# Optimization experiments

Hardware: AMD Instinct MI355X
Metric: run time of the kernel (lower is better)

The kernel has to match this reference:

```python
import jax, jax.numpy as jnp
import numpy as np

# Model dims
C = 16          # in_channels / d_model
D_INNER = 64    # expand * C, expand = 64 // C = 4
HEADDIM = 4
NHEADS = D_INNER // HEADDIM   # 16
D_STATE = 64
D_CONV = 4
CONV_DIM = D_INNER + 2 * D_STATE        # 192 (x, B, C streams)
D_IN_PROJ = 2 * D_INNER + 2 * D_STATE + NHEADS  # 272 (z, xBC, dt)
# Input volume
BSZ, DD, HH, WW = 8, 32, 16, 16
L = DD * HH * WW  # 8192, multiple of 256 -> exact adaptive max pool
POOL = 256


def setup_inputs():
    key = jax.random.key(0)
    ks = jax.random.split(key, 10)
    x = jax.random.normal(ks[0], (BSZ, C, DD, HH, WW), jnp.float32)
    # 3 independent Mamba2 blocks -> stack params with leading dim 3
    Win = jax.random.normal(ks[1], (3, D_IN_PROJ, C), jnp.float32) / np.sqrt(C).astype(np.float32)
    conv_w = jax.random.normal(ks[2], (3, CONV_DIM, D_CONV), jnp.float32) / np.sqrt(D_CONV).astype(np.float32)
    conv_b = jax.random.normal(ks[3], (3, CONV_DIM), jnp.float32) * 0.1
    dt_bias = jax.random.normal(ks[4], (3, NHEADS), jnp.float32) * 0.5
    A_log = jnp.log(jax.random.uniform(ks[5], (3, NHEADS), jnp.float32, minval=1.0, maxval=16.0))
    Dp = jax.random.normal(ks[6], (3, NHEADS), jnp.float32) * 0.5 + 1.0
    norm_w = jnp.ones((3, D_INNER), jnp.float32)
    Wout = jax.random.normal(ks[7], (3, C, D_INNER), jnp.float32) / np.sqrt(D_INNER).astype(np.float32)
    gamma = jnp.ones((3, C), jnp.float32)
    beta = jnp.zeros((3, C), jnp.float32)
    lin_w = jax.random.normal(ks[8], (3, 1, C), jnp.float32) / np.sqrt(C).astype(np.float32)
    lin_b = jnp.zeros((3, 1), jnp.float32)
    return dict(x=x, Win=Win, conv_w=conv_w, conv_b=conv_b, dt_bias=dt_bias,
                A_log=A_log, Dp=Dp, norm_w=norm_w, Wout=Wout,
                gamma=gamma, beta=beta, lin_w=lin_w, lin_b=lin_b)


def _mamba2(u, Win, conv_w, conv_b, dt_bias, A_log, Dp, norm_w, Wout):
    """Mamba2 block: u (B, L, C) -> (B, L, C). ngroups=1, rmsnorm gated."""
    B, Lx, _ = u.shape
    zxbcdt = jnp.einsum('blc,pc->blp', u, Win)  # (B, L, 272)
    z = zxbcdt[..., :D_INNER]
    xBC = zxbcdt[..., D_INNER:D_INNER + CONV_DIM]
    dt = jax.nn.softplus(zxbcdt[..., D_INNER + CONV_DIM:] + dt_bias)  # (B, L, H)
    # causal depthwise conv over time
    conv = jax.lax.conv_general_dilated(
        jnp.transpose(xBC, (0, 2, 1)), conv_w[:, None, :], (1,),
        [(D_CONV - 1, 0)], feature_group_count=CONV_DIM)
    xBC = jax.nn.silu(jnp.transpose(conv, (0, 2, 1)) + conv_b)
    xh = xBC[..., :D_INNER].reshape(B, Lx, NHEADS, HEADDIM)
    Bm = xBC[..., D_INNER:D_INNER + D_STATE]   # (B, L, N)
    Cm = xBC[..., D_INNER + D_STATE:]          # (B, L, N)
    A = -jnp.exp(A_log)                        # (H,)
    dA = jnp.exp(dt * A)                       # (B, L, H)
    dtx = dt[..., None] * xh                   # (B, L, H, P)

    def step(S, inp):
        dA_t, dtx_t, B_t, C_t = inp
        S = S * dA_t[:, :, None, None] + dtx_t[..., None] * B_t[:, None, None, :]
        y_t = jnp.einsum('bhpn,bn->bhp', S, C_t)
        return S, y_t

    S0 = jnp.zeros((B, NHEADS, HEADDIM, D_STATE), u.dtype)
    xs = (jnp.moveaxis(dA, 1, 0), jnp.moveaxis(dtx, 1, 0),
          jnp.moveaxis(Bm, 1, 0), jnp.moveaxis(Cm, 1, 0))
    _, ys = jax.lax.scan(step, S0, xs)                       # (L, B, H, P)
    y = jnp.moveaxis(ys, 0, 1) + Dp[None, None, :, None] * xh
    y = y.reshape(B, Lx, D_INNER) * jax.nn.silu(z)           # gate first
    y = y * jax.lax.rsqrt(jnp.mean(y * y, -1, keepdims=True) + 1e-5) * norm_w
    return jnp.einsum('bld,cd->blc', y, Wout)


def _proj_pool(y, gamma, beta, lw, lb):
    """ReLU -> BatchNorm1d (batch stats) -> Linear(C,1) -> AdaptiveMaxPool1d(256)."""
    B, Lx, _ = y.shape
    v = jax.nn.relu(y.reshape(-1, C))
    mu = jnp.mean(v, 0)
    var = jnp.mean((v - mu) ** 2, 0)
    v = (v - mu) * jax.lax.rsqrt(var + 1e-5) * gamma + beta
    s = (v @ lw.T + lb).reshape(B, Lx)
    return jnp.max(s.reshape(B, POOL, Lx // POOL), -1)  # (B, 256)


def reference(x, Win, conv_w, conv_b, dt_bias, A_log, Dp, norm_w, Wout,
              gamma, beta, lin_w, lin_b):
    B, Cc, Dd, Hh, Ww = x.shape
    Lx = Dd * Hh * Ww
    fD = jnp.transpose(x.reshape(B, Cc, Lx), (0, 2, 1))
    fH = jnp.transpose(jnp.transpose(x, (0, 1, 3, 4, 2)).reshape(B, Cc, Lx), (0, 2, 1))
    fW = jnp.transpose(jnp.transpose(x, (0, 1, 4, 2, 3)).reshape(B, Cc, Lx), (0, 2, 1))
    seqs = jnp.stack([fD, fH, fW], 0)  # (3, B, L, C)
    ys = jax.vmap(_mamba2)(seqs, Win, conv_w, conv_b, dt_bias, A_log, Dp, norm_w, Wout)
    pooled = jax.vmap(_proj_pool)(ys, gamma, beta, lin_w, lin_b)  # (3, B, 256)
    return jnp.concatenate([pooled[0], pooled[1], pooled[2]], -1)[:, None, :]  # (B,1,768)
```

## Files before the change

kernel.cpp:

```cpp
#include <hip/hip_runtime.h>
#include <math.h>

#define CONVD 192
#define NC 128
#define PW 32
#define LOG2E 1.4426950408889634f
#define LN2f  0.69314718055994531f

#define OFF_DST   0u
#define OFF_CHA   4194304u
#define OFF_YS    4210688u
#define OFF_PART  5259264u
#define PD        5292032u

#define XSW(m, t)   ((m) * 64 + (((((t) >> 2) ^ ((m) & 15)) & 15) << 2) + ((t) & 3))
#define XSW4(m, tq) ((m) * 64 + ((((tq) ^ ((m) & 15)) & 15) << 2))

__device__ __forceinline__ float fast_silu(float x) {
    float e = __builtin_amdgcn_exp2f(-x * LOG2E);
    return x * __builtin_amdgcn_rcpf(1.f + e);
}
__device__ __forceinline__ float fast_softplus(float x) {
    if (x > 20.f) return x;
    float e = __builtin_amdgcn_exp2f(x * LOG2E);
    return LN2f * __builtin_amdgcn_logf(1.f + e);
}

template<int NT>
__device__ __forceinline__ void stage_u(
    const float* __restrict__ x, float* u_s, int b, int l0, int dir, int tid)
{
    for (int i = tid; i < 67 * 16; i += NT) {
        int pos = i >> 4, c = i & 15;
        int l = l0 + pos - 3;
        float v = 0.f;
        if (l >= 0) {
            if (dir == 0) {
                v = x[(b * 16 + c) * 8192 + l];
            } else if (dir == 1) {
                int h = l >> 9, w = (l >> 5) & 15, d = l & 31;
                v = x[(((b * 16 + c) * 32 + d) * 16 + h) * 16 + w];
            } else {
                int w = l >> 9, d = (l >> 4) & 31, h = l & 15;
                v = x[(((b * 16 + c) * 32 + d) * 16 + h) * 16 + w];
            }
        }
        u_s[pos * 17 + c] = v;
    }
}

__global__ __launch_bounds__(512, 6) void k_delta(
    const float* __restrict__ x, const float* __restrict__ Win,
    const float* __restrict__ convw, const float* __restrict__ convb,
    const float* __restrict__ dtb, const float* __restrict__ A_log,
    float* __restrict__ ws, int dir0, int dslm)
{
    __shared__ float u_s[67 * 17];
    __shared__ float xh_c[4096];
    __shared__ float Bs[4096];
    __shared__ float dts[16 * 65];
    __shared__ float wbuf[16 * 65];
    const int tid = threadIdx.x;
    const int ck = blockIdx.x;
    const int b = blockIdx.y;
    const int dir = dir0 + blockIdx.z;
    float* base = ws + (size_t)(dslm * blockIdx.z) * PD;
    float* Dst = base + OFF_DST;
    float* chA = base + OFF_CHA;
    const int l0 = ck * 64;

    stage_u<512>(x, u_s, b, l0, dir, tid);
    __syncthreads();

    const int lane = tid & 63;
    const int wv = __builtin_amdgcn_readfirstlane(tid >> 6);

    float u[16], uh[16];
    {
        const float* ur = &u_s[(lane + 3) * 17];
        #pragma unroll
        for (int k = 0; k < 16; k++) u[k] = ur[k];
        const float* uhr = &u_s[(lane < 3 ? lane : 0) * 17];
        #pragma unroll
        for (int k = 0; k < 16; k++) uh[k] = uhr[k];
    }

    for (int i = 0; i < 18; i++) {
        const int g = wv * 18 + i;
        const int col = (g < 128) ? (64 + g) : (256 + (g - 128));
        const float* wp = Win + (size_t)(dir * 272 + col) * 16;
        float acc = 0.f, hacc = 0.f;
        #pragma unroll
        for (int k = 0; k < 16; k++) {
            acc += u[k] * wp[k];
            hacc += uh[k] * wp[k];
        }
        if (col < 256) {
            const int ch = col - 64;
            float v1 = __shfl_up(acc, 1);
            float v2 = __shfl_up(acc, 2);
            float v3 = __shfl_up(acc, 3);
            float h0 = __shfl(hacc, 0);
            float h1 = __shfl(hacc, 1);
            float h2 = __shfl(hacc, 2);
            float m1 = (lane >= 1) ? v1 : h2;
            float m2 = (lane >= 2) ? v2 : ((lane == 0) ? h1 : h2);
            float m3 = (lane >= 3) ? v3 : ((lane == 0) ? h0 : ((lane == 1) ? h1 : h2));
            const float* cwp = convw + (size_t)(dir * CONVD + ch) * 4;
            float conv = convb[dir * CONVD + ch]
                       + cwp[0] * m3 + cwp[1] * m2 + cwp[2] * m1 + cwp[3] * acc;
            float xv = fast_silu(conv);
            if (ch < 64) xh_c[XSW(ch, lane)] = xv;
            else         Bs[XSW(ch - 64, lane)] = xv;
        } else {
            const int h = col - 256;
            dts[h * 65 + lane] = fast_softplus(acc + dtb[dir * 16 + h]);
        }
    }
    __syncthreads();

    for (int h = wv; h < 16; h += 8) {
        float A2 = -expf(A_log[dir * 16 + h]) * LOG2E;
        float dtv = dts[h * 65 + lane];
        float v = dtv * A2;
        #pragma unroll
        for (int off = 1; off < 64; off <<= 1) {
            float o = __shfl_up(v, off, 64);
            if (lane >= off) v += o;
        }
        float tot = __shfl(v, 63, 64);
        wbuf[h * 65 + lane] = __builtin_amdgcn_exp2f(tot - v) * dtv;
        if (lane == 63) chA[(b * 16 + h) * 128 + ck] = __builtin_amdgcn_exp2f(tot);
    }
    __syncthreads();

    for (int j = tid; j < 4096; j += 512) {
        int hp = j >> 6, t = j & 63;
        xh_c[XSW(hp, t)] *= wbuf[(hp >> 2) * 65 + t];
    }
    __syncthreads();

    if (tid < 256) {
        const int hp4 = tid >> 4, n4 = tid & 15;
        float a[4][4] = {};
        for (int tq = 0; tq < 16; tq++) {
            float4 xv[4], bv[4];
            #pragma unroll
            for (int i2 = 0; i2 < 4; i2++) {
                xv[i2] = *(const float4*)&xh_c[XSW4(4 * hp4 + i2, tq)];
                bv[i2] = *(const float4*)&Bs[XSW4(4 * n4 + i2, tq)];
            }
            #pragma unroll
            for (int i2 = 0; i2 < 4; i2++)
                #pragma unroll
                for (int j2 = 0; j2 < 4; j2++)
                    a[i2][j2] += xv[i2].x * bv[j2].x + xv[i2].y * bv[j2].y
                               + xv[i2].z * bv[j2].z + xv[i2].w * bv[j2].w;
        }
        #pragma unroll
        for (int i2 = 0; i2 < 4; i2++) {
            int hp = 4 * hp4 + i2;
            int h = hp >> 2, p = hp & 3;
            *(float4*)(Dst + ((size_t)((b * 16 + h) * 128 + ck)) * 256 + p * 64 + 4 * n4) =
                make_float4(a[i2][0], a[i2][1], a[i2][2], a[i2][3]);
        }
    }
}

__global__ __launch_bounds__(64) void k_chunk_scan(
    float* __restrict__ ws, int dslm)
{
    float* base = ws + (size_t)(dslm * blockIdx.z) * PD;
    float* Dst = base + OFF_DST;
    const float* chA = base + OFF_CHA;
    const int bh = blockIdx.x >> 2;
    const int elem = (blockIdx.x & 3) * 64 + threadIdx.x;
    float S = 0.f;
    for (int k0 = 0; k0 < NC; k0 += 8) {
        float d[8], av[8];
        #pragma unroll
        for (int j = 0; j < 8; j++) {
            d[j] = Dst[((size_t)(bh * 128 + k0 + j)) * 256 + elem];
            av[j] = chA[bh * 128 + k0 + j];
        }
        #pragma unroll
        for (int j = 0; j < 8; j++) {
            Dst[((size_t)(bh * 128 + k0 + j)) * 256 + elem] = S;
            S = av[j] * S + d[j];
        }
    }
}

__global__ __launch_bounds__(512, 4) void k_out_epi(
    const float* __restrict__ x, const float* __restrict__ Win,
    const float* __restrict__ convw, const float* __restrict__ convb,
    const float* __restrict__ dtb, const float* __restrict__ A_log,
    const float* __restrict__ Dp, const float* __restrict__ normw,
    const float* __restrict__ Wout, float* __restrict__ ws, int dir0, int dslm)
{
    __shared__ float SinT[64 * 65];
    __shared__ float xh_c[4096];
    __shared__ float Bz[4096];
    __shared__ float Cy[4352];
    __shared__ float uW[67 * 17];
    __shared__ float dts[16 * 68];
    __shared__ float ct2l[16 * 68];
    __shared__ float Dps[16];
    __shared__ float red[4][34];
    float* base = ws + (size_t)(dslm * blockIdx.z) * PD;
    const float* Dst = base + OFF_DST;
    float* ys        = base + OFF_YS;
    float* partials  = base + OFF_PART;
    const int dir = dir0 + blockIdx.z;
    const int tid = threadIdx.x;
    const int b = blockIdx.y;
    const int ck = blockIdx.x;
    const int l0 = ck * 64;
    const int tg = tid & 255;
    const int t4 = tg >> 4, x4 = tg & 15;
    const int grp = tid >> 8;
    const int lane = tid & 63;
    const int wv = __builtin_amdgcn_readfirstlane(tid >> 6);

    stage_u<512>(x, uW, b, l0, dir, tid);
    for (int j = tid; j < 1024; j += 512) {
        int hp = j >> 4, n4 = (j & 15) << 2;
        int h = hp >> 2, p = hp & 3;
        float4 sv = *(const float4*)(Dst + ((size_t)((b * 16 + h) * 128 + ck)) * 256 + p * 64 + n4);
        SinT[(n4 + 0) * 65 + hp] = sv.x;
        SinT[(n4 + 1) * 65 + hp] = sv.y;
        SinT[(n4 + 2) * 65 + hp] = sv.z;
        SinT[(n4 + 3) * 65 + hp] = sv.w;
    }
    if (tid < 16) Dps[tid] = Dp[dir * 16 + tid];
    __syncthreads();

    float u[16], uh[16];
    {
        const float* ur = &uW[(lane + 3) * 17];
        #pragma unroll
        for (int k = 0; k < 16; k++) u[k] = ur[k];
        const float* uhr = &uW[(lane < 3 ? lane : 0) * 17];
        #pragma unroll
        for (int k = 0; k < 16; k++) uh[k] = uhr[k];
    }

    for (int i = 0; i < 26; i++) {
        const int col = 64 + wv * 26 + i;
        const float* wp = Win + (size_t)(dir * 272 + col) * 16;
        float acc = 0.f, hacc = 0.f;
        #pragma unroll
        for (int k = 0; k < 16; k++) {
            acc += u[k] * wp[k];
            hacc += uh[k] * wp[k];
        }
        if (col < 256) {
            const int ch = col - 64;
            float v1 = __shfl_up(acc, 1);
            float v2 = __shfl_up(acc, 2);
            float v3 = __shfl_up(acc, 3);
            float h0 = __shfl(hacc, 0);
            float h1 = __shfl(hacc, 1);
            float h2 = __shfl(hacc, 2);
            float m1 = (lane >= 1) ? v1 : h2;
            float m2 = (lane >= 2) ? v2 : ((lane == 0) ? h1 : h2);
            float m3 = (lane >= 3) ? v3 : ((lane == 0) ? h0 : ((lane == 1) ? h1 : h2));
            const float* cwp = convw + (size_t)(dir * CONVD + ch) * 4;
            float conv = convb[dir * CONVD + ch]
                       + cwp[0] * m3 + cwp[1] * m2 + cwp[2] * m1 + cwp[3] * acc;
            float xv = fast_silu(conv);
            if (ch < 64)       xh_c[XSW(ch, lane)] = xv;
            else if (ch < 128) Bz[XSW(ch - 64, lane)] = xv;
            else               Cy[XSW(ch - 128, lane)] = xv;
        } else {
            const int h = col - 256;
            dts[h * 68 + lane] = fast_softplus(acc + dtb[dir * 16 + h]);
        }
    }
    __syncthreads();

    for (int h = wv; h < 16; h += 8) {
        float A2 = -expf(A_log[dir * 16 + h]) * LOG2E;
        float dtv = dts[h * 68 + lane];
        float v = dtv * A2;
        #pragma unroll
        for (int off = 1; off < 64; off <<= 1) {
            float o = __shfl_up(v, off, 64);
            if (lane >= off) v += o;
        }
        ct2l[h * 68 + lane] = v;
    }
    __syncthreads();

    float G_[4][4] = {}, CS_[4][4] = {};
    if (grp == 0) {
        for (int n = 0; n < 64; n++) {
            float4 cr4 = *(const float4*)&Cy[XSW4(n, t4)];
            float4 br4 = *(const float4*)&Bz[XSW4(n, x4)];
            float cr[4] = {cr4.x, cr4.y, cr4.z, cr4.w};
            float br[4] = {br4.x, br4.y, br4.z, br4.w};
            #pragma unroll
            for (int r = 0; r < 4; r++)
                #pragma unroll
                for (int q = 0; q < 4; q++)
                    G_[r][q] += cr[r] * br[q];
        }
    } else {
        for (int n = 0; n < 64; n++) {
            float4 cr4 = *(const float4*)&Cy[XSW4(n, t4)];
            float cr[4] = {cr4.x, cr4.y, cr4.z, cr4.w};
            float sn[4];
            #pragma unroll
            for (int q = 0; q < 4; q++) sn[q] = SinT[n * 65 + 4 * x4 + q];
            #pragma unroll
            for (int r = 0; r < 4; r++)
                #pragma unroll
                for (int q = 0; q < 4; q++)
                    CS_[r][q] += cr[r] * sn[q];
        }
    }
    __syncthreads();

    if (grp == 0) {
        #pragma unroll
        for (int k = 0; k < 16; k++) Cy[k * 257 + tg] = G_[k >> 2][k & 3];
    } else if (x4 < 8) {
        const int idx = t4 * 8 + x4;
        #pragma unroll
        for (int k = 0; k < 16; k++) SinT[k * 129 + idx] = CS_[k >> 2][k & 3];
    }
    __syncthreads();
    if (grp == 1) {
        #pragma unroll
        for (int k = 0; k < 16; k++) G_[k >> 2][k & 3] = Cy[k * 257 + tg];
    } else if (x4 < 8) {
        const int idx = t4 * 8 + x4;
        #pragma unroll
        for (int k = 0; k < 16; k++) CS_[k >> 2][k & 3] = SinT[k * 129 + idx];
    }

    for (int i = 0; i < 8; i++) {
        const int col = wv * 8 + i;
        const float* wp = Win + (size_t)(dir * 272 + col) * 16;
        float acc = 0.f;
        #pragma unroll
        for (int k = 0; k < 16; k++) acc += u[k] * wp[k];
        Bz[XSW(col, lane)] = acc;
    }
    for (int j = tid; j < 1024; j += 512) {
        int c = j >> 6, d = j & 63;
        uW[c * 65 + d] = Wout[dir * 1024 + j] * normw[dir * 64 + d];
    }
    __syncthreads();

    float* yv = Cy;
    const int tbase = 4 * t4;
    #pragma unroll 1
    for (int hh = 0; hh < 8; hh++) {
        const int h = 8 * grp + hh;
        const float* ctp = &ct2l[h * 68];
        const float* dtp = &dts[h * 68];
        float4 ctt4 = *(const float4*)&ctp[tbase];
        const float ctt[4] = {ctt4.x, ctt4.y, ctt4.z, ctt4.w};
        float ect[4];
        #pragma unroll
        for (int r = 0; r < 4; r++) ect[r] = __builtin_amdgcn_exp2f(ctt[r]);
        float4 cs4 = *(const float4*)&ctp[4 * x4];
        float4 dt4 = *(const float4*)&dtp[4 * x4];
        float v[16] = {0.f, 0.f, 0.f, 0.f, 0.f, 0.f, 0.f, 0.f,
                       0.f, 0.f, 0.f, 0.f, 0.f, 0.f, 0.f, 0.f};
        #pragma unroll
        for (int q = 0; q < 4; q++) {
            const int s = 4 * x4 + q;
            float csq = (q == 0) ? cs4.x : (q == 1) ? cs4.y : (q == 2) ? cs4.z : cs4.w;
            float dtq = (q == 0) ? dt4.x : (q == 1) ? dt4.y : (q == 2) ? dt4.z : dt4.w;
            float xv[4];
            #pragma unroll
            for (int p = 0; p < 4; p++) {
                int m = 4 * h + p;
                xv[p] = xh_c[m * 64 + (((x4 ^ (m & 15)) & 15) << 2) + q];
            }
            #pragma unroll
            for (int r = 0; r < 4; r++) {
                float e = __builtin_amdgcn_exp2f(ctt[r] - csq);
                float w = (s <= tbase + r) ? (G_[r][q] * dtq) * e : 0.f;
                #pragma unroll
                for (int p = 0; p < 4; p++) v[4 * r + p] += w * xv[p];
            }
        }
        if (x4 == h) {
            #pragma unroll
            for (int r = 0; r < 4; r++)
                #pragma unroll
                for (int p = 0; p < 4; p++)
                    v[4 * r + p] += ect[r] * CS_[r][p];
        }
        #pragma unroll
        for (int j = 0; j < 8; j++) {
            float a = (x4 & 8) ? v[j + 8] : v[j];
            float s_ = (x4 & 8) ? v[j] : v[j + 8];
            v[j] = a + __shfl_xor(s_, 8);
        }
        #pragma unroll
        for (int j = 0; j < 4; j++) {
            float a = (x4 & 4) ? v[j + 4] : v[j];
            float s_ = (x4 & 4) ? v[j] : v[j + 4];
            v[j] = a + __shfl_xor(s_, 4);
        }
        #pragma unroll
        for (int j = 0; j < 2; j++) {
            float a = (x4 & 2) ? v[j + 2] : v[j];
            float s_ = (x4 & 2) ? v[j] : v[j + 2];
            v[j] = a + __shfl_xor(s_, 2);
        }
        {
            float a = (x4 & 1) ? v[1] : v[0];
            float s_ = (x4 & 1) ? v[0] : v[1];
            v[0] = a + __shfl_xor(s_, 1);
        }
        const int row = tbase + (x4 >> 2);
        yv[(row * 4 + (x4 & 3)) * 17 + h] = v[0];
    }
    __syncthreads();

    float os[4];
    const int row = tid >> 2;
    const int p = tid & 3;
    if (tid < 256) {
        float gg[16], sumsq = 0.f;
        #pragma unroll
        for (int h = 0; h < 16; h++) {
            float yval = yv[(row * 4 + p) * 17 + h];
            int m = 4 * h + p;
            int ax = m * 64 + ((((row >> 2) ^ (m & 15)) & 15) << 2) + (row & 3);
            float xh = xh_c[ax];
            float zv = Bz[ax];
            float val = (yval + Dps[h] * xh) * fast_silu(zv);
            gg[h] = val;
            sumsq += val * val;
        }
        sumsq += __shfl_xor(sumsq, 1);
        sumsq += __shfl_xor(sumsq, 2);
        float rms = rsqrtf(sumsq * (1.f / 64.f) + 1e-5f);

        float oc[16];
        #pragma unroll
        for (int c = 0; c < 16; c++) {
            float a = 0.f;
            #pragma unroll
            for (int h = 0; h < 16; h++) a += gg[h] * uW[c * 65 + 4 * h + p];
            oc[c] = a;
        }
        #pragma unroll
        for (int c = 0; c < 16; c++) {
            oc[c] += __shfl_xor(oc[c], 1);
            oc[c] += __shfl_xor(oc[c], 2);
        }
        #pragma unroll
        for (int i2 = 0; i2 < 4; i2++) {
            float a0 = (p == 0) ? oc[i2] : oc[4 + i2];
            float a1 = (p == 2) ? oc[8 + i2] : oc[12 + i2];
            os[i2] = (((p & 2) == 0) ? a0 : a1) * rms;
        }
        size_t bl = (size_t)(b * 8192 + l0 + row);
        *(float4*)(ys + bl * 16 + 4 * p) = make_float4(os[0], os[1], os[2], os[3]);

        float bs[4], bq[4];
        #pragma unroll
        for (int i2 = 0; i2 < 4; i2++) {
            float vv = fmaxf(os[i2], 0.f);
            bs[i2] = vv;
            bq[i2] = vv * vv;
        }
        #pragma unroll
        for (int off = 4; off < 64; off <<= 1) {
            #pragma unroll
            for (int i2 = 0; i2 < 4; i2++) {
                bs[i2] += __shfl_xor(bs[i2], off);
                bq[i2] += __shfl_xor(bq[i2], off);
            }
        }
        const int wlane = tid & 63, wvid = tid >> 6;
        if (wlane < 4) {
            #pragma unroll
// ... 69 lines not shown
        m = fmaxf(m, sv);
    }
    m = fmaxf(m, __shfl_xor(m, 1));
    m = fmaxf(m, __shfl_xor(m, 2));
    m = fmaxf(m, __shfl_xor(m, 4));
    if (sub == 0) out[b * 768 + dir * 256 + j] = m;
}

extern "C" void kernel_launch(void* const* d_in, const int* in_sizes, int n_in,
                              void* d_out, int out_size, void* d_ws, size_t ws_size,
                              hipStream_t stream) {
    const float* x     = (const float*)d_in[0];
    const float* Win   = (const float*)d_in[1];
    const float* convw = (const float*)d_in[2];
    const float* convb = (const float*)d_in[3];
    const float* dtb   = (const float*)d_in[4];
    const float* Alog  = (const float*)d_in[5];
    const float* Dp    = (const float*)d_in[6];
    const float* normw = (const float*)d_in[7];
    const float* Wout  = (const float*)d_in[8];
    const float* gamma = (const float*)d_in[9];
    const float* beta  = (const float*)d_in[10];
    const float* linw  = (const float*)d_in[11];
    const float* linb  = (const float*)d_in[12];
    float* out = (float*)d_out;
    float* ws = (float*)d_ws;

    const bool batched = ws_size >= (size_t)3 * PD * 4;
    const int nz = batched ? 3 : 1;
    const int dslm = batched ? 1 : 0;
    const int nloop = batched ? 1 : 3;

    for (int d0 = 0; d0 < nloop; ++d0) {
        k_delta<<<dim3(128, 8, nz), dim3(512), 0, stream>>>(
            x, Win, convw, convb, dtb, Alog, ws, d0, dslm);
        k_chunk_scan<<<dim3(512, 1, nz), dim3(64), 0, stream>>>(ws, dslm);
        k_out_epi<<<dim3(128, 8, nz), dim3(512), 0, stream>>>(
            x, Win, convw, convb, dtb, Alog, Dp, normw, Wout, ws, d0, dslm);
        k_pool_bn<<<dim3(64, 1, nz), dim3(256), 0, stream>>>(
            gamma, beta, linw, linb, ws, out, d0, dslm);
    }
}
```

Before: 356.1 us.

## Use packed FP32 FMAs and precompute conv halo once per block

Rewrites the per-lane dot products, outer-product accumulations and the output projection with v_pk_fma_f32 inline asm, so each instruction does two FP32 FMAs. The causal-conv halo projections are now computed once per block by a subset of threads into shared memory, instead of every lane computing a second halo dot product per column. Shared-memory layouts for SinT and the Wout tile are changed to allow vectorised reads. This adds extra barriers and inline asm that the compiler cannot schedule around, and it changes the order of floating-point sums.

```diff
diff --git a/kernel.cpp b/kernel.cpp
--- a/kernel.cpp
+++ b/kernel.cpp
@@ -15,6 +15,36 @@
 
 #define XSW(m, t)   ((m) * 64 + (((((t) >> 2) ^ ((m) & 15)) & 15) << 2) + ((t) & 3))
 #define XSW4(m, tq) ((m) * 64 + ((((tq) ^ ((m) & 15)) & 15) << 2))
+
+typedef float f32x2 __attribute__((ext_vector_type(2)));
+
+__device__ __forceinline__ f32x2 pk_fma(f32x2 a, f32x2 b, f32x2 c) {
+    f32x2 d;
+    asm("v_pk_fma_f32 %0, %1, %2, %3" : "=v"(d) : "v"(a), "v"(b), "v"(c));
+    return d;
+}
+__device__ __forceinline__ f32x2 pk_fma_alo(f32x2 a, f32x2 b, f32x2 c) {
+    f32x2 d;
+    asm("v_pk_fma_f32 %0, %1, %2, %3 op_sel_hi:[0,1,1]" : "=v"(d) : "v"(a), "v"(b), "v"(c));
+    return d;
+}
+__device__ __forceinline__ f32x2 pk_fma_ahi(f32x2 a, f32x2 b, f32x2 c) {
+    f32x2 d;
+    asm("v_pk_fma_f32 %0, %1, %2, %3 op_sel:[1,0,0]" : "=v"(d) : "v"(a), "v"(b), "v"(c));
+    return d;
+}
+__device__ __forceinline__ f32x2 pk_fma_blo(f32x2 a, f32x2 b, f32x2 c) {
+    f32x2 d;
+    asm("v_pk_fma_f32 %0, %1, %2, %3 op_sel_hi:[1,0,1]" : "=v"(d) : "v"(a), "v"(b), "v"(c));
+    return d;
+}
+__device__ __forceinline__ f32x2 pk_fma_bhi(f32x2 a, f32x2 b, f32x2 c) {
+    f32x2 d;
+    asm("v_pk_fma_f32 %0, %1, %2, %3 op_sel:[0,1,0]" : "=v"(d) : "v"(a), "v"(b), "v"(c));
+    return d;
+}
+__device__ __forceinline__ f32x2 lo2(float4 v) { f32x2 r; r.x = v.x; r.y = v.y; return r; }
+__device__ __forceinline__ f32x2 hi2(float4 v) { f32x2 r; r.x = v.z; r.y = v.w; return r; }
 
 __device__ __forceinline__ float fast_silu(float x) {
     float e = __builtin_amdgcn_exp2f(-x * LOG2E);
@@ -47,6 +77,23 @@
         }
         u_s[pos * 17 + c] = v;
     }
+}
+
+__device__ __forceinline__ float pk_dot16(const f32x2* u2, const float* wp) {
+    float4 w0 = *(const float4*)(wp);
+    float4 w1 = *(const float4*)(wp + 4);
+    float4 w2 = *(const float4*)(wp + 8);
+    float4 w3 = *(const float4*)(wp + 12);
+    f32x2 a = {0.f, 0.f};
+    a = pk_fma(u2[0], lo2(w0), a);
+    a = pk_fma(u2[1], hi2(w0), a);
+    a = pk_fma(u2[2], lo2(w1), a);
+    a = pk_fma(u2[3], hi2(w1), a);
+    a = pk_fma(u2[4], lo2(w2), a);
+    a = pk_fma(u2[5], hi2(w2), a);
+    a = pk_fma(u2[6], lo2(w3), a);
+    a = pk_fma(u2[7], hi2(w3), a);
+    return a.x + a.y;
 }
 
 __global__ __launch_bounds__(512, 6) void k_delta(
@@ -68,6 +115,7 @@
     float* Dst = base + OFF_DST;
     float* chA = base + OFF_CHA;
     const int l0 = ck * 64;
+    float* halo = wbuf;
 
     stage_u<512>(x, u_s, b, l0, dir, tid);
     __syncthreads();
@@ -75,37 +123,39 @@
     const int lane = tid & 63;
     const int wv = __builtin_amdgcn_readfirstlane(tid >> 6);
 
-    float u[16], uh[16];
+    f32x2 u2[8];
     {
         const float* ur = &u_s[(lane + 3) * 17];
         #pragma unroll
-        for (int k = 0; k < 16; k++) u[k] = ur[k];
-        const float* uhr = &u_s[(lane < 3 ? lane : 0) * 17];
-        #pragma unroll
-        for (int k = 0; k < 16; k++) uh[k] = uhr[k];
-    }
+        for (int k = 0; k < 8; k++) { u2[k].x = ur[2 * k]; u2[k].y = ur[2 * k + 1]; }
+    }
+    if (tid < 128) {
+        f32x2 uh2[8];
+        #pragma unroll
+        for (int pos = 0; pos < 3; pos++) {
+            const float* uhr = &u_s[pos * 17];
+            #pragma unroll
+            for (int k = 0; k < 8; k++) { uh2[k].x = uhr[2 * k]; uh2[k].y = uhr[2 * k + 1]; }
+            halo[pos * 128 + tid] = pk_dot16(uh2, Win + (size_t)(dir * 272 + 64 + tid) * 16);
+        }
+    }
+    __syncthreads();
 
     for (int i = 0; i < 18; i++) {
         const int g = wv * 18 + i;
         const int col = (g < 128) ? (64 + g) : (256 + (g - 128));
-        const float* wp = Win + (size_t)(dir * 272 + col) * 16;
-        float acc = 0.f, hacc = 0.f;
-        #pragma unroll
-        for (int k = 0; k < 16; k++) {
-            acc += u[k] * wp[k];
-            hacc += uh[k] * wp[k];
-        }
+        float acc = pk_dot16(u2, Win + (size_t)(dir * 272 + col) * 16);
         if (col < 256) {
             const int ch = col - 64;
             float v1 = __shfl_up(acc, 1);
             float v2 = __shfl_up(acc, 2);
             float v3 = __shfl_up(acc, 3);
-            float h0 = __shfl(hacc, 0);
-            float h1 = __shfl(hacc, 1);
-            float h2 = __shfl(hacc, 2);
-            float m1 = (lane >= 1) ? v1 : h2;
-            float m2 = (lane >= 2) ? v2 : ((lane == 0) ? h1 : h2);
-            float m3 = (lane >= 3) ? v3 : ((lane == 0) ? h0 : ((lane == 1) ? h1 : h2));
+            float hh0 = halo[ch];
+            float hh1 = halo[128 + ch];
+            float hh2 = halo[256 + ch];
+            float m1 = (lane >= 1) ? v1 : hh2;
+            float m2 = (lane >= 2) ? v2 : ((lane == 0) ? hh1 : hh2);
+            float m3 = (lane >= 3) ? v3 : ((lane == 0) ? hh0 : ((lane == 1) ? hh1 : hh2));
             const float* cwp = convw + (size_t)(dir * CONVD + ch) * 4;
             float conv = convb[dir * CONVD + ch]
                        + cwp[0] * m3 + cwp[1] * m2 + cwp[2] * m1 + cwp[3] * acc;
@@ -142,7 +192,7 @@
 
     if (tid < 256) {
         const int hp4 = tid >> 4, n4 = tid & 15;
-        float a[4][4] = {};
+        f32x2 a2[4][4] = {};
         for (int tq = 0; tq < 16; tq++) {
             float4 xv[4], bv[4];
             #pragma unroll
@@ -153,16 +203,18 @@
             #pragma unroll
             for (int i2 = 0; i2 < 4; i2++)
                 #pragma unroll
-                for (int j2 = 0; j2 < 4; j2++)
-                    a[i2][j2] += xv[i2].x * bv[j2].x + xv[i2].y * bv[j2].y
-                               + xv[i2].z * bv[j2].z + xv[i2].w * bv[j2].w;
+                for (int j2 = 0; j2 < 4; j2++) {
+                    a2[i2][j2] = pk_fma(lo2(xv[i2]), lo2(bv[j2]), a2[i2][j2]);
+                    a2[i2][j2] = pk_fma(hi2(xv[i2]), hi2(bv[j2]), a2[i2][j2]);
+                }
         }
         #pragma unroll
         for (int i2 = 0; i2 < 4; i2++) {
             int hp = 4 * hp4 + i2;
             int h = hp >> 2, p = hp & 3;
             *(float4*)(Dst + ((size_t)((b * 16 + h) * 128 + ck)) * 256 + p * 64 + 4 * n4) =
-                make_float4(a[i2][0], a[i2][1], a[i2][2], a[i2][3]);
+                make_float4(a2[i2][0].x + a2[i2][0].y, a2[i2][1].x + a2[i2][1].y,
+                            a2[i2][2].x + a2[i2][2].y, a2[i2][3].x + a2[i2][3].y);
         }
     }
 }
@@ -198,7 +250,7 @@
     const float* __restrict__ Dp, const float* __restrict__ normw,
     const float* __restrict__ Wout, float* __restrict__ ws, int dir0, int dslm)
 {
-    __shared__ float SinT[64 * 65];
+    __shared__ float SinT[64 * 66];
     __shared__ float xh_c[4096];
     __shared__ float Bz[4096];
     __shared__ float Cy[4352];
@@ -221,50 +273,53 @@
     const int grp = tid >> 8;
     const int lane = tid & 63;
     const int wv = __builtin_amdgcn_readfirstlane(tid >> 6);
+    float* halo = ct2l;
 
     stage_u<512>(x, uW, b, l0, dir, tid);
     for (int j = tid; j < 1024; j += 512) {
         int hp = j >> 4, n4 = (j & 15) << 2;
         int h = hp >> 2, p = hp & 3;
         float4 sv = *(const float4*)(Dst + ((size_t)((b * 16 + h) * 128 + ck)) * 256 + p * 64 + n4);
-        SinT[(n4 + 0) * 65 + hp] = sv.x;
-        SinT[(n4 + 1) * 65 + hp] = sv.y;
-        SinT[(n4 + 2) * 65 + hp] = sv.z;
-        SinT[(n4 + 3) * 65 + hp] = sv.w;
+        SinT[(n4 + 0) * 66 + hp] = sv.x;
+        SinT[(n4 + 1) * 66 + hp] = sv.y;
+        SinT[(n4 + 2) * 66 + hp] = sv.z;
+        SinT[(n4 + 3) * 66 + hp] = sv.w;
     }
     if (tid < 16) Dps[tid] = Dp[dir * 16 + tid];
     __syncthreads();
 
-    float u[16], uh[16];
+    f32x2 u2[8];
     {
         const float* ur = &uW[(lane + 3) * 17];
         #pragma unroll
-        for (int k = 0; k < 16; k++) u[k] = ur[k];
-        const float* uhr = &uW[(lane < 3 ? lane : 0) * 17];
-        #pragma unroll
-        for (int k = 0; k < 16; k++) uh[k] = uhr[k];
-    }
+        for (int k = 0; k < 8; k++) { u2[k].x = ur[2 * k]; u2[k].y = ur[2 * k + 1]; }
+    }
+    if (tid < 192) {
+        f32x2 uh2[8];
+        #pragma unroll
+        for (int pos = 0; pos < 3; pos++) {
+            const float* uhr = &uW[pos * 17];
+            #pragma unroll
+            for (int k = 0; k < 8; k++) { uh2[k].x = uhr[2 * k]; uh2[k].y = uhr[2 * k + 1]; }
+            halo[pos * 192 + tid] = pk_dot16(uh2, Win + (size_t)(dir * 272 + 64 + tid) * 16);
+        }
+    }
+    __syncthreads();
 
     for (int i = 0; i < 26; i++) {
         const int col = 64 + wv * 26 + i;
-        const float* wp = Win + (size_t)(dir * 272 + col) * 16;
-        float acc = 0.f, hacc = 0.f;
-        #pragma unroll
-        for (int k = 0; k < 16; k++) {
-            acc += u[k] * wp[k];
-            hacc += uh[k] * wp[k];
-        }
+        float acc = pk_dot16(u2, Win + (size_t)(dir * 272 + col) * 16);
         if (col < 256) {
             const int ch = col - 64;
             float v1 = __shfl_up(acc, 1);
             float v2 = __shfl_up(acc, 2);
             float v3 = __shfl_up(acc, 3);
-            float h0 = __shfl(hacc, 0);
-            float h1 = __shfl(hacc, 1);
-            float h2 = __shfl(hacc, 2);
-            float m1 = (lane >= 1) ? v1 : h2;
-            float m2 = (lane >= 2) ? v2 : ((lane == 0) ? h1 : h2);
-            float m3 = (lane >= 3) ? v3 : ((lane == 0) ? h0 : ((lane == 1) ? h1 : h2));
+            float hh0 = halo[ch];
+            float hh1 = halo[192 + ch];
+            float hh2 = halo[384 + ch];
+            float m1 = (lane >= 1) ? v1 : hh2;
+            float m2 = (lane >= 2) ? v2 : ((lane == 0) ? hh1 : hh2);
+            float m3 = (lane >= 3) ? v3 : ((lane == 0) ? hh0 : ((lane == 1) ? hh1 : hh2));
             const float* cwp = convw + (size_t)(dir * CONVD + ch) * 4;
             float conv = convb[dir * CONVD + ch]
                        + cwp[0] * m3 + cwp[1] * m2 + cwp[2] * m1 + cwp[3] * acc;
@@ -292,31 +347,40 @@
     }
     __syncthreads();
 
-    float G_[4][4] = {}, CS_[4][4] = {};
+    float G_[4][4], CS_[4][4];
     if (grp == 0) {
+        f32x2 G2[4][2] = {};
         for (int n = 0; n < 64; n++) {
             float4 cr4 = *(const float4*)&Cy[XSW4(n, t4)];
             float4 br4 = *(const float4*)&Bz[XSW4(n, x4)];
-            float cr[4] = {cr4.x, cr4.y, cr4.z, cr4.w};
-            float br[4] = {br4.x, br4.y, br4.z, br4.w};
-            #pragma unroll
-            for (int r = 0; r < 4; r++)
-                #pragma unroll
-                for (int q = 0; q < 4; q++)
-                    G_[r][q] += cr[r] * br[q];
+            f32x2 c01 = lo2(cr4), c23 = hi2(cr4);
+            f32x2 b01 = lo2(br4), b23 = hi2(br4);
+            G2[0][0] = pk_fma_alo(c01, b01, G2[0][0]); G2[0][1] = pk_fma_alo(c01, b23, G2[0][1]);
+            G2[1][0] = pk_fma_ahi(c01, b01, G2[1][0]); G2[1][1] = pk_fma_ahi(c01, b23, G2[1][1]);
+            G2[2][0] = pk_fma_alo(c23, b01, G2[2][0]); G2[2][1] = pk_fma_alo(c23, b23, G2[2][1]);
+            G2[3][0] = pk_fma_ahi(c23, b01, G2[3][0]); G2[3][1] = pk_fma_ahi(c23, b23, G2[3][1]);
+        }
+        #pragma unroll
+        for (int r = 0; r < 4; r++) {
+            G_[r][0] = G2[r][0].x; G_[r][1] = G2[r][0].y;
+            G_[r][2] = G2[r][1].x; G_[r][3] = G2[r][1].y;
         }
     } else {
+        f32x2 C2[4][2] = {};
         for (int n = 0; n < 64; n++) {
             float4 cr4 = *(const float4*)&Cy[XSW4(n, t4)];
-            float cr[4] = {cr4.x, cr4.y, cr4.z, cr4.w};
-            float sn[4];
-            #pragma unroll
-            for (int q = 0; q < 4; q++) sn[q] = SinT[n * 65 + 4 * x4 + q];
-            #pragma unroll
-            for (int r = 0; r < 4; r++)
-                #pragma unroll
-                for (int q = 0; q < 4; q++)
-                    CS_[r][q] += cr[r] * sn[q];
+            f32x2 c01 = lo2(cr4), c23 = hi2(cr4);
+            f32x2 s01 = *(const f32x2*)&SinT[n * 66 + 4 * x4];
+            f32x2 s23 = *(const f32x2*)&SinT[n * 66 + 4 * x4 + 2];
+            C2[0][0] = pk_fma_alo(c01, s01, C2[0][0]); C2[0][1] = pk_fma_alo(c01, s23, C2[0][1]);
+            C2[1][0] = pk_fma_ahi(c01, s01, C2[1][0]); C2[1][1] = pk_fma_ahi(c01, s23, C2[1][1]);
+            C2[2][0] = pk_fma_alo(c23, s01, C2[2][0]); C2[2][1] = pk_fma_alo(c23, s23, C2[2][1]);
+            C2[3][0] = pk_fma_ahi(c23, s01, C2[3][0]); C2[3][1] = pk_fma_ahi(c23, s23, C2[3][1]);
+        }
+        #pragma unroll
+        for (int r = 0; r < 4; r++) {
+            CS_[r][0] = C2[r][0].x; CS_[r][1] = C2[r][0].y;
+            CS_[r][2] = C2[r][1].x; CS_[r][3] = C2[r][1].y;
         }
     }
     __syncthreads();
@@ -341,15 +405,13 @@
 
     for (int i = 0; i < 8; i++) {
         const int col = wv * 8 + i;
-        const float* wp = Win + (size_t)(dir * 272 + col) * 16;
-        float acc = 0.f;
-        #pragma unroll
-        for (int k = 0; k < 16; k++) acc += u[k] * wp[k];
+        float acc = pk_dot16(u2, Win + (size_t)(dir * 272 + col) * 16);
         Bz[XSW(col, lane)] = acc;
     }
     for (int j = tid; j < 1024; j += 512) {
         int c = j >> 6, d = j & 63;
-        uW[c * 65 + d] = Wout[dir * 1024 + j] * normw[dir * 64 + d];
+        float val = Wout[dir * 1024 + j] * normw[dir * 64 + d];
+        uW[(d & 3) * 256 + c * 16 + (d >> 2)] = val;
     }
     __syncthreads();
 
@@ -362,38 +424,59 @@
         const float* dtp = &dts[h * 68];
         float4 ctt4 = *(const float4*)&ctp[tbase];
         const float ctt[4] = {ctt4.x, ctt4.y, ctt4.z, ctt4.w};
-        float ect[4];
-        #pragma unroll
-        for (int r = 0; r < 4; r++) ect[r] = __builtin_amdgcn_exp2f(ctt[r]);
         float4 cs4 = *(const float4*)&ctp[4 * x4];
         float4 dt4 = *(const float4*)&dtp[4 * x4];
-        float v[16] = {0.f, 0.f, 0.f, 0.f, 0.f, 0.f, 0.f, 0.f,
-                       0.f, 0.f, 0.f, 0.f, 0.f, 0.f, 0.f, 0.f};
+        float4 xq[4];
+        #pragma unroll
+        for (int p = 0; p < 4; p++) {
+            int m = 4 * h + p;
+            xq[p] = *(const float4*)&xh_c[m * 64 + (((x4 ^ (m & 15)) & 15) << 2)];
+        }
+        f32x2 v2[2][4] = {};
         #pragma unroll
         for (int q = 0; q < 4; q++) {
             const int s = 4 * x4 + q;
             float csq = (q == 0) ? cs4.x : (q == 1) ? cs4.y : (q == 2) ? cs4.z : cs4.w;
             float dtq = (q == 0) ? dt4.x : (q == 1) ? dt4.y : (q == 2) ? dt4.z : dt4.w;
-            float xv[4];
-            #pragma unroll
-            for (int p = 0; p < 4; p++) {
-                int m = 4 * h + p;
-                xv[p] = xh_c[m * 64 + (((x4 ^ (m & 15)) & 15) << 2) + q];
-            }
+            float w[4];
             #pragma unroll
             for (int r = 0; r < 4; r++) {
                 float e = __builtin_amdgcn_exp2f(ctt[r] - csq);
-                float w = (s <= tbase + r) ? (G_[r][q] * dtq) * e : 0.f;
-                #pragma unroll
-                for (int p = 0; p < 4; p++) v[4 * r + p] += w * xv[p];
+                w[r] = (s <= tbase + r) ? (G_[r][q] * dtq) * e : 0.f;
             }
+            f32x2 wp0 = {w[0], w[1]};
+            f32x2 wp1 = {w[2], w[3]};
+            #pragma unroll
+            for (int p = 0; p < 4; p++) {
+                f32x2 xpair = (q < 2) ? lo2(xq[p]) : hi2(xq[p]);
+                if (q & 1) {
+                    v2[0][p] = pk_fma_bhi(wp0, xpair, v2[0][p]);
+                    v2[1][p] = pk_fma_bhi(wp1, xpair, v2[1][p]);
+                } else {
+                    v2[0][p] = pk_fma_blo(wp0, xpair, v2[0][p]);
+                    v2[1][p] = pk_fma_blo(wp1, xpair, v2[1][p]);
+                }
+            }
         }
         if (x4 == h) {
-            #pragma unroll
-            for (int r = 0; r < 4; r++)
-                #pragma unroll
-                for (int p = 0; p < 4; p++)
-                    v[4 * r + p] += ect[r] * CS_[r][p];
+            float ect[4];
+            #pragma unroll
+            for (int r = 0; r < 4; r++) ect[r] = __builtin_amdgcn_exp2f(ctt[r]);
+            #pragma unroll
+            for (int p = 0; p < 4; p++) {
+                v2[0][p].x += ect[0] * CS_[0][p];
+                v2[0][p].y += ect[1] * CS_[1][p];
+                v2[1][p].x += ect[2] * CS_[2][p];
+                v2[1][p].y += ect[3] * CS_[3][p];
+            }
+        }
+        float v[16];
+        #pragma unroll
+        for (int p = 0; p < 4; p++) {
+            v[p]      = v2[0][p].x;
+            v[4 + p]  = v2[0][p].y;
+            v[8 + p]  = v2[1][p].x;
+            v[12 + p] = v2[1][p].y;
         }
         #pragma unroll
         for (int j = 0; j < 8; j++) {
@@ -443,13 +526,27 @@
         sumsq += __shfl_xor(sumsq, 2);
         float rms = rsqrtf(sumsq * (1.f / 64.f) + 1e-5f);
 
+        f32x2 gg2[8];
+        #pragma unroll
+        for (int k = 0; k < 8; k++) { gg2[k].x = gg[2 * k]; gg2[k].y = gg[2 * k + 1]; }
+        const float* WoN = uW + p * 256;
         float oc[16];
         #pragma unroll
         for (int c = 0; c < 16; c++) {
-            float a = 0.f;
-            #pragma unroll
-            for (int h = 0; h < 16; h++) a += gg[h] * uW[c * 65 + 4 * h + p];
-            oc[c] = a;
+            float4 wa = *(const float4*)&WoN[c * 16];
+            float4 wb = *(const float4*)&WoN[c * 16 + 4];
+            float4 wc = *(const float4*)&WoN[c * 16 + 8];
+            float4 wd = *(const float4*)&WoN[c * 16 + 12];
+            f32x2 a = {0.f, 0.f};
+            a = pk_fma(gg2[0], lo2(wa), a);
+            a = pk_fma(gg2[1], hi2(wa), a);
+            a = pk_fma(gg2[2], lo2(wb), a);
+            a = pk_fma(gg2[3], hi2(wb), a);
+            a = pk_fma(gg2[4], lo2(wc), a);
+            a = pk_fma(gg2[5], hi2(wc), a);
+            a = pk_fma(gg2[6], lo2(wd), a);
+            a = pk_fma(gg2[7], hi2(wd), a);
+            oc[c] = a.x + a.y;
         }
         #pragma unroll
         for (int c = 0; c < 16; c++) {
```

After: 358.3 us. About the same (+0.6%).

## Reuse front-kernel conv, dt and Gram results in epilogue via workspace tiles

Applied to the files above, without the earlier changes.

The front kernel now also computes the C stream, the C·Bᵀ Gram matrix and the dt cumsum, and writes x, C, G, dt and the cumsum per chunk to a new workspace region. The epilogue loads these instead of recomputing the input projection, the convolution and the Gram matrix. The C·S product is split across both thread groups with a partial-sum exchange. Dot products use packed FMA, and the halo projection is computed once per block instead of per wave. The cost is a much larger workspace and extra global traffic, plus lower occupancy hints (512,2).

```diff
diff --git a/kernel.cpp b/kernel.cpp
--- a/kernel.cpp
+++ b/kernel.cpp
@@ -11,10 +11,27 @@
 #define OFF_CHA   4194304u
 #define OFF_YS    4210688u
 #define OFF_PART  5259264u
-#define PD        5292032u
+#define OFF_TILE  5267456u
+#define PD        19947520u
+
+#define TXH 0
+#define TC  4096
+#define TG  8192
+#define TDT 12288
+#define TCT 13312
 
 #define XSW(m, t)   ((m) * 64 + (((((t) >> 2) ^ ((m) & 15)) & 15) << 2) + ((t) & 3))
 #define XSW4(m, tq) ((m) * 64 + ((((tq) ^ ((m) & 15)) & 15) << 2))
+
+typedef float f32x2 __attribute__((ext_vector_type(2)));
+
+__device__ __forceinline__ f32x2 pk_fma(f32x2 a, f32x2 b, f32x2 c) {
+    f32x2 d;
+    asm("v_pk_fma_f32 %0, %1, %2, %3" : "=v"(d) : "v"(a), "v"(b), "v"(c));
+    return d;
+}
+__device__ __forceinline__ f32x2 lo2(float4 v) { f32x2 r; r.x = v.x; r.y = v.y; return r; }
+__device__ __forceinline__ f32x2 hi2(float4 v) { f32x2 r; r.x = v.z; r.y = v.w; return r; }
 
 __device__ __forceinline__ float fast_silu(float x) {
     float e = __builtin_amdgcn_exp2f(-x * LOG2E);
@@ -49,7 +66,24 @@
     }
 }
 
-__global__ __launch_bounds__(512, 6) void k_delta(
+__device__ __forceinline__ float pk_dot16(const f32x2* u2, const float* wp) {
+    float4 w0 = *(const float4*)(wp);
+    float4 w1 = *(const float4*)(wp + 4);
+    float4 w2 = *(const float4*)(wp + 8);
+    float4 w3 = *(const float4*)(wp + 12);
+    f32x2 a = {0.f, 0.f};
+    a = pk_fma(u2[0], lo2(w0), a);
+    a = pk_fma(u2[1], hi2(w0), a);
+    a = pk_fma(u2[2], lo2(w1), a);
+    a = pk_fma(u2[3], hi2(w1), a);
+    a = pk_fma(u2[4], lo2(w2), a);
+    a = pk_fma(u2[5], hi2(w2), a);
+    a = pk_fma(u2[6], lo2(w3), a);
+    a = pk_fma(u2[7], hi2(w3), a);
+    return a.x + a.y;
+}
+
+__global__ __launch_bounds__(512, 2) void k_front(
     const float* __restrict__ x, const float* __restrict__ Win,
     const float* __restrict__ convw, const float* __restrict__ convb,
     const float* __restrict__ dtb, const float* __restrict__ A_log,
@@ -58,6 +92,7 @@
     __shared__ float u_s[67 * 17];
     __shared__ float xh_c[4096];
     __shared__ float Bs[4096];
+    __shared__ float Cc[4096];
     __shared__ float dts[16 * 65];
     __shared__ float wbuf[16 * 65];
     const int tid = threadIdx.x;
@@ -67,7 +102,9 @@
     float* base = ws + (size_t)(dslm * blockIdx.z) * PD;
     float* Dst = base + OFF_DST;
     float* chA = base + OFF_CHA;
+    float* tile = base + OFF_TILE + (size_t)(b * 128 + ck) * 14336;
     const int l0 = ck * 64;
+    float* halo = wbuf;
 
     stage_u<512>(x, u_s, b, l0, dir, tid);
     __syncthreads();
@@ -75,50 +112,58 @@
     const int lane = tid & 63;
     const int wv = __builtin_amdgcn_readfirstlane(tid >> 6);
 
-    float u[16], uh[16];
+    f32x2 u2[8];
     {
         const float* ur = &u_s[(lane + 3) * 17];
         #pragma unroll
-        for (int k = 0; k < 16; k++) u[k] = ur[k];
-        const float* uhr = &u_s[(lane < 3 ? lane : 0) * 17];
-        #pragma unroll
-        for (int k = 0; k < 16; k++) uh[k] = uhr[k];
-    }
-
-    for (int i = 0; i < 18; i++) {
-        const int g = wv * 18 + i;
-        const int col = (g < 128) ? (64 + g) : (256 + (g - 128));
-        const float* wp = Win + (size_t)(dir * 272 + col) * 16;
-        float acc = 0.f, hacc = 0.f;
-        #pragma unroll
-        for (int k = 0; k < 16; k++) {
-            acc += u[k] * wp[k];
-            hacc += uh[k] * wp[k];
-        }
+        for (int k = 0; k < 8; k++) { u2[k].x = ur[2 * k]; u2[k].y = ur[2 * k + 1]; }
+    }
+    if (tid < 192) {
+        f32x2 uh2[8];
+        #pragma unroll
+        for (int pos = 0; pos < 3; pos++) {
+            const float* uhr = &u_s[pos * 17];
+            #pragma unroll
+            for (int k = 0; k < 8; k++) { uh2[k].x = uhr[2 * k]; uh2[k].y = uhr[2 * k + 1]; }
+            halo[pos * 192 + tid] = pk_dot16(uh2, Win + (size_t)(dir * 272 + 64 + tid) * 16);
+        }
+    }
+    __syncthreads();
+
+    for (int i = 0; i < 26; i++) {
+        const int col = 64 + wv * 26 + i;
+        float acc = pk_dot16(u2, Win + (size_t)(dir * 272 + col) * 16);
         if (col < 256) {
             const int ch = col - 64;
             float v1 = __shfl_up(acc, 1);
             float v2 = __shfl_up(acc, 2);
             float v3 = __shfl_up(acc, 3);
-            float h0 = __shfl(hacc, 0);
-            float h1 = __shfl(hacc, 1);
-            float h2 = __shfl(hacc, 2);
-            float m1 = (lane >= 1) ? v1 : h2;
-            float m2 = (lane >= 2) ? v2 : ((lane == 0) ? h1 : h2);
-            float m3 = (lane >= 3) ? v3 : ((lane == 0) ? h0 : ((lane == 1) ? h1 : h2));
+            float hh0 = halo[ch];
+            float hh1 = halo[192 + ch];
+            float hh2 = halo[384 + ch];
+            float m1 = (lane >= 1) ? v1 : hh2;
+            float m2 = (lane >= 2) ? v2 : ((lane == 0) ? hh1 : hh2);
+            float m3 = (lane >= 3) ? v3 : ((lane == 0) ? hh0 : ((lane == 1) ? hh1 : hh2));
             const float* cwp = convw + (size_t)(dir * CONVD + ch) * 4;
             float conv = convb[dir * CONVD + ch]
                        + cwp[0] * m3 + cwp[1] * m2 + cwp[2] * m1 + cwp[3] * acc;
             float xv = fast_silu(conv);
-            if (ch < 64) xh_c[XSW(ch, lane)] = xv;
-            else         Bs[XSW(ch - 64, lane)] = xv;
+            if (ch < 64)       xh_c[XSW(ch, lane)] = xv;
+            else if (ch < 128) Bs[XSW(ch - 64, lane)] = xv;
+            else               Cc[XSW(ch - 128, lane)] = xv;
         } else {
             const int h = col - 256;
-            dts[h * 65 + lane] = fast_softplus(acc + dtb[dir * 16 + h]);
-        }
-    }
-    __syncthreads();
-
+            float dv = fast_softplus(acc + dtb[dir * 16 + h]);
+            dts[h * 65 + lane] = dv;
+            tile[TDT + h * 64 + lane] = dv;
+        }
+    }
+    __syncthreads();
+
+    for (int j4 = tid; j4 < 1024; j4 += 512) {
+        ((float4*)(tile + TXH))[j4] = ((const float4*)xh_c)[j4];
+        ((float4*)(tile + TC))[j4]  = ((const float4*)Cc)[j4];
+    }
     for (int h = wv; h < 16; h += 8) {
         float A2 = -expf(A_log[dir * 16 + h]) * LOG2E;
         float dtv = dts[h * 65 + lane];
@@ -129,6 +174,7 @@
             if (lane >= off) v += o;
         }
         float tot = __shfl(v, 63, 64);
+        tile[TCT + h * 64 + lane] = v;
         wbuf[h * 65 + lane] = __builtin_amdgcn_exp2f(tot - v) * dtv;
         if (lane == 63) chA[(b * 16 + h) * 128 + ck] = __builtin_amdgcn_exp2f(tot);
     }
@@ -142,7 +188,7 @@
 
     if (tid < 256) {
         const int hp4 = tid >> 4, n4 = tid & 15;
-        float a[4][4] = {};
+        f32x2 a2[4][4] = {};
         for (int tq = 0; tq < 16; tq++) {
             float4 xv[4], bv[4];
             #pragma unroll
@@ -153,17 +199,38 @@
             #pragma unroll
             for (int i2 = 0; i2 < 4; i2++)
                 #pragma unroll
-                for (int j2 = 0; j2 < 4; j2++)
-                    a[i2][j2] += xv[i2].x * bv[j2].x + xv[i2].y * bv[j2].y
-                               + xv[i2].z * bv[j2].z + xv[i2].w * bv[j2].w;
+                for (int j2 = 0; j2 < 4; j2++) {
+                    a2[i2][j2] = pk_fma(lo2(xv[i2]), lo2(bv[j2]), a2[i2][j2]);
+                    a2[i2][j2] = pk_fma(hi2(xv[i2]), hi2(bv[j2]), a2[i2][j2]);
+                }
         }
         #pragma unroll
         for (int i2 = 0; i2 < 4; i2++) {
             int hp = 4 * hp4 + i2;
             int h = hp >> 2, p = hp & 3;
             *(float4*)(Dst + ((size_t)((b * 16 + h) * 128 + ck)) * 256 + p * 64 + 4 * n4) =
-                make_float4(a[i2][0], a[i2][1], a[i2][2], a[i2][3]);
-        }
+                make_float4(a2[i2][0].x + a2[i2][0].y, a2[i2][1].x + a2[i2][1].y,
+                            a2[i2][2].x + a2[i2][2].y, a2[i2][3].x + a2[i2][3].y);
+        }
+    } else {
+        const int tg2 = tid - 256;
+        const int t4g = tg2 >> 4, x4g = tg2 & 15;
+        float G_[4][4] = {};
+        for (int n = 0; n < 64; n++) {
+            float4 cr4 = *(const float4*)&Cc[XSW4(n, t4g)];
+            float4 br4 = *(const float4*)&Bs[XSW4(n, x4g)];
+            float cr[4] = {cr4.x, cr4.y, cr4.z, cr4.w};
+            float br[4] = {br4.x, br4.y, br4.z, br4.w};
+            #pragma unroll
+            for (int r = 0; r < 4; r++)
+                #pragma unroll
+                for (int q = 0; q < 4; q++)
+                    G_[r][q] += cr[r] * br[q];
+        }
+        float* gdst = tile + TG + (size_t)tg2 * 16;
+        #pragma unroll
+        for (int r = 0; r < 4; r++)
+            *(float4*)(gdst + 4 * r) = make_float4(G_[r][0], G_[r][1], G_[r][2], G_[r][3]);
     }
 }
 
@@ -191,14 +258,12 @@
     }
 }
 
-__global__ __launch_bounds__(512, 4) void k_out_epi(
+__global__ __launch_bounds__(512, 2) void k_out_epi(
     const float* __restrict__ x, const float* __restrict__ Win,
-    const float* __restrict__ convw, const float* __restrict__ convb,
-    const float* __restrict__ dtb, const float* __restrict__ A_log,
     const float* __restrict__ Dp, const float* __restrict__ normw,
     const float* __restrict__ Wout, float* __restrict__ ws, int dir0, int dslm)
 {
-    __shared__ float SinT[64 * 65];
+    __shared__ float SinT[64 * 68];
     __shared__ float xh_c[4096];
     __shared__ float Bz[4096];
     __shared__ float Cy[4352];
@@ -211,6 +276,7 @@
     const float* Dst = base + OFF_DST;
     float* ys        = base + OFF_YS;
     float* partials  = base + OFF_PART;
+    const float* tile = base + OFF_TILE + (size_t)(blockIdx.y * 128 + blockIdx.x) * 14336;
     const int dir = dir0 + blockIdx.z;
     const int tid = threadIdx.x;
     const int b = blockIdx.y;
@@ -223,95 +289,55 @@
     const int wv = __builtin_amdgcn_readfirstlane(tid >> 6);
 
     stage_u<512>(x, uW, b, l0, dir, tid);
+    for (int j4 = tid; j4 < 1024; j4 += 512) {
+        ((float4*)xh_c)[j4] = ((const float4*)(tile + TXH))[j4];
+        ((float4*)Cy)[j4]   = ((const float4*)(tile + TC))[j4];
+    }
+    if (tid < 256) {
+        int h = tid >> 4, tq = tid & 15;
+        *(float4*)&dts[h * 68 + 4 * tq]  = ((const float4*)(tile + TDT))[tid];
+        *(float4*)&ct2l[h * 68 + 4 * tq] = ((const float4*)(tile + TCT))[tid];
+    }
     for (int j = tid; j < 1024; j += 512) {
         int hp = j >> 4, n4 = (j & 15) << 2;
         int h = hp >> 2, p = hp & 3;
         float4 sv = *(const float4*)(Dst + ((size_t)((b * 16 + h) * 128 + ck)) * 256 + p * 64 + n4);
-        SinT[(n4 + 0) * 65 + hp] = sv.x;
-        SinT[(n4 + 1) * 65 + hp] = sv.y;
-        SinT[(n4 + 2) * 65 + hp] = sv.z;
-        SinT[(n4 + 3) * 65 + hp] = sv.w;
+        SinT[(n4 + 0) * 68 + hp] = sv.x;
+        SinT[(n4 + 1) * 68 + hp] = sv.y;
+        SinT[(n4 + 2) * 68 + hp] = sv.z;
+        SinT[(n4 + 3) * 68 + hp] = sv.w;
+    }
+    float G_[4][4];
+    {
+        const float* gsrc = tile + TG + (size_t)tg * 16;
+        #pragma unroll
+        for (int r = 0; r < 4; r++) {
+            float4 g4 = *(const float4*)(gsrc + 4 * r);
+            G_[r][0] = g4.x; G_[r][1] = g4.y; G_[r][2] = g4.z; G_[r][3] = g4.w;
+        }
     }
     if (tid < 16) Dps[tid] = Dp[dir * 16 + tid];
     __syncthreads();
 
-    float u[16], uh[16];
     {
+        f32x2 u2[8];
         const float* ur = &uW[(lane + 3) * 17];
         #pragma unroll
-        for (int k = 0; k < 16; k++) u[k] = ur[k];
-        const float* uhr = &uW[(lane < 3 ? lane : 0) * 17];
-        #pragma unroll
-        for (int k = 0; k < 16; k++) uh[k] = uhr[k];
-    }
-
-    for (int i = 0; i < 26; i++) {
-        const int col = 64 + wv * 26 + i;
-        const float* wp = Win + (size_t)(dir * 272 + col) * 16;
-        float acc = 0.f, hacc = 0.f;
-        #pragma unroll
-        for (int k = 0; k < 16; k++) {
-            acc += u[k] * wp[k];
-            hacc += uh[k] * wp[k];
-        }
-        if (col < 256) {
-            const int ch = col - 64;
-            float v1 = __shfl_up(acc, 1);
-            float v2 = __shfl_up(acc, 2);
-            float v3 = __shfl_up(acc, 3);
-            float h0 = __shfl(hacc, 0);
-            float h1 = __shfl(hacc, 1);
-            float h2 = __shfl(hacc, 2);
-            float m1 = (lane >= 1) ? v1 : h2;
-            float m2 = (lane >= 2) ? v2 : ((lane == 0) ? h1 : h2);
-            float m3 = (lane >= 3) ? v3 : ((lane == 0) ? h0 : ((lane == 1) ? h1 : h2));
-            const float* cwp = convw + (size_t)(dir * CONVD + ch) * 4;
-            float conv = convb[dir * CONVD + ch]
-                       + cwp[0] * m3 + cwp[1] * m2 + cwp[2] * m1 + cwp[3] * acc;
-            float xv = fast_silu(conv);
-            if (ch < 64)       xh_c[XSW(ch, lane)] = xv;
-            else if (ch < 128) Bz[XSW(ch - 64, lane)] = xv;
-            else               Cy[XSW(ch - 128, lane)] = xv;
-        } else {
-            const int h = col - 256;
-            dts[h * 68 + lane] = fast_softplus(acc + dtb[dir * 16 + h]);
-        }
-    }
-    __syncthreads();
-
-    for (int h = wv; h < 16; h += 8) {
-        float A2 = -expf(A_log[dir * 16 + h]) * LOG2E;
-        float dtv = dts[h * 68 + lane];
-        float v = dtv * A2;
-        #pragma unroll
-        for (int off = 1; off < 64; off <<= 1) {
-            float o = __shfl_up(v, off, 64);
-            if (lane >= off) v += o;
-        }
-        ct2l[h * 68 + lane] = v;
-    }
-    __syncthreads();
-
-    float G_[4][4] = {}, CS_[4][4] = {};
-    if (grp == 0) {
-        for (int n = 0; n < 64; n++) {
-            float4 cr4 = *(const float4*)&Cy[XSW4(n, t4)];
-            float4 br4 = *(const float4*)&Bz[XSW4(n, x4)];
-            float cr[4] = {cr4.x, cr4.y, cr4.z, cr4.w};
-            float br[4] = {br4.x, br4.y, br4.z, br4.w};
-            #pragma unroll
-            for (int r = 0; r < 4; r++)
-                #pragma unroll
-                for (int q = 0; q < 4; q++)
-                    G_[r][q] += cr[r] * br[q];
-        }
-    } else {
-        for (int n = 0; n < 64; n++) {
+        for (int k = 0; k < 8; k++) { u2[k].x = ur[2 * k]; u2[k].y = ur[2 * k + 1]; }
+        for (int i = 0; i < 8; i++) {
+            const int col = wv * 8 + i;
+            Bz[XSW(col, lane)] = pk_dot16(u2, Win + (size_t)(dir * 272 + col) * 16);
+        }
+    }
+    float CS_[4][4] = {};
+    {
+        const int n0 = grp << 5;
+        for (int n = n0; n < n0 + 32; n++) {
             float4 cr4 = *(const float4*)&Cy[XSW4(n, t4)];
             float cr[4] = {cr4.x, cr4.y, cr4.z, cr4.w};
             float sn[4];
             #pragma unroll
-            for (int q = 0; q < 4; q++) sn[q] = SinT[n * 65 + 4 * x4 + q];
+            for (int q = 0; q < 4; q++) sn[q] = SinT[n * 68 + 4 * x4 + q];
             #pragma unroll
             for (int r = 0; r < 4; r++)
                 #pragma unroll
@@ -321,35 +347,20 @@
     }
     __syncthreads();
 
-    if (grp == 0) {
-        #pragma unroll
-        for (int k = 0; k < 16; k++) Cy[k * 257 + tg] = G_[k >> 2][k & 3];
-    } else if (x4 < 8) {
-        const int idx = t4 * 8 + x4;
-        #pragma unroll
-        for (int k = 0; k < 16; k++) SinT[k * 129 + idx] = CS_[k >> 2][k & 3];
-    }
-    __syncthreads();
-    if (grp == 1) {
-        #pragma unroll
-        for (int k = 0; k < 16; k++) G_[k >> 2][k & 3] = Cy[k * 257 + tg];
-    } else if (x4 < 8) {
-        const int idx = t4 * 8 + x4;
-        #pragma unroll
-        for (int k = 0; k < 16; k++) CS_[k >> 2][k & 3] = SinT[k * 129 + idx];
-    }
-
-    for (int i = 0; i < 8; i++) {
-        const int col = wv * 8 + i;
-        const float* wp = Win + (size_t)(dir * 272 + col) * 16;
-        float acc = 0.f;
-        #pragma unroll
-        for (int k = 0; k < 16; k++) acc += u[k] * wp[k];
-        Bz[XSW(col, lane)] = acc;
+    {
+        float* ex = (grp == 0) ? SinT : Cy;
+        #pragma unroll
+        for (int k = 0; k < 16; k++) ex[tg * 17 + k] = CS_[k >> 2][k & 3];
     }
     for (int j = tid; j < 1024; j += 512) {
         int c = j >> 6, d = j & 63;
         uW[c * 65 + d] = Wout[dir * 1024 + j] * normw[dir * 64 + d];
+    }
+    __syncthreads();
+    {
+        const float* ex = (grp == 0) ? Cy : SinT;
+        #pragma unroll
+        for (int k = 0; k < 16; k++) CS_[k >> 2][k & 3] += ex[tg * 17 + k];
     }
     __syncthreads();
 
@@ -585,11 +596,11 @@
     const int nloop = batched ? 1 : 3;
 
     for (int d0 = 0; d0 < nloop; ++d0) {
-        k_delta<<<dim3(128, 8, nz), dim3(512), 0, stream>>>(
+        k_front<<<dim3(128, 8, nz), dim3(512), 0, stream>>>(
             x, Win, convw, convb, dtb, Alog, ws, d0, dslm);
         k_chunk_scan<<<dim3(512, 1, nz), dim3(64), 0, stream>>>(ws, dslm);
         k_out_epi<<<dim3(128, 8, nz), dim3(512), 0, stream>>>(
-            x, Win, convw, convb, dtb, Alog, Dp, normw, Wout, ws, d0, dslm);
+            x, Win, Dp, normw, Wout, ws, d0, dslm);
         k_pool_bn<<<dim3(64, 1, nz), dim3(256), 0, stream>>>(
             gamma, beta, linw, linb, ws, out, d0, dslm);
     }
```

New measurement: 386.8 us. 1.09x slower.
